# Performance work log

Measured on AMD Instinct MI355X. Metric: run time of the kernel, lower is better.

Reference implementation:

```python
import jax, jax.numpy as jnp
import numpy as np

C = 1.0          # Poincare ball curvature
NORM_FACTOR = 1.0
EPS = 1e-7
MAX_NORM = (1.0 - 1e-5) / np.sqrt(C)


def _artanh(x):
    x = jnp.clip(x, -1.0 + EPS, 1.0 - EPS)
    return jnp.arctanh(x)


def logmap0(x):
    # tangent vector at origin of Poincare ball (c=C)
    n = jnp.clip(jnp.linalg.norm(x, axis=-1, keepdims=True), EPS, None)
    sc = np.sqrt(C)
    return _artanh(sc * n) * x / (sc * n)


def expmap0(u):
    n = jnp.clip(jnp.linalg.norm(u, axis=-1, keepdims=True), EPS, None)
    sc = np.sqrt(C)
    return jnp.tanh(sc * n) * u / (sc * n)


def proj(x):
    # clip points to stay strictly inside the ball
    n = jnp.clip(jnp.linalg.norm(x, axis=-1, keepdims=True), EPS, None)
    return jnp.where(n > MAX_NORM, x / n * MAX_NORM, x)


def setup_inputs() -> dict:
    key = jax.random.key(0)
    ks = jax.random.split(key, 10)
    B, N, D_IN, D_H, D_LAT, L = 32, 1024, 128, 128, 64, 2
    s_in = 1.0 / np.sqrt(D_IN)
    s_h = 1.0 / np.sqrt(D_H)
    return {
        "node_features": jax.random.normal(ks[0], (B, N, D_IN), jnp.float32),
        "adjacency_matrix": jax.random.uniform(ks[1], (B, N, N), jnp.float32),
        "node_mask": jnp.ones((B, N, 1), jnp.float32),
        "W_embed": jax.random.normal(ks[2], (D_H, D_IN), jnp.float32) * s_in,
        "W_msg": jax.random.normal(ks[3], (L, D_H, D_H), jnp.float32) * s_h,
        "b_msg": jnp.zeros((L, D_H), jnp.float32),
        "W_agg": jax.random.normal(ks[4], (L, D_H, D_H), jnp.float32) * s_h,
        "b_agg": jnp.zeros((L, D_H), jnp.float32),
        "W_proj": jax.random.normal(ks[5], (2 * D_LAT, D_H), jnp.float32) * s_h,
        "b_proj": jnp.zeros((2 * D_LAT,), jnp.float32),
    }


def reference(node_features, adjacency_matrix, node_mask,
              W_embed, W_msg, b_msg, W_agg, b_agg, W_proj, b_proj):
    # feature embedding (bias-free linear, weights live on the manifold);
    # map to the Poincare ball
    h = jnp.einsum('bnd,hd->bnh', node_features, W_embed)
    x = proj(expmap0(h))

    num_layers = W_msg.shape[0]
    for l in range(num_layers):  # small fixed layer count
        t = logmap0(x)                                   # [B,N,D]
        m = t @ W_msg[l] + b_msg[l]                      # message transform
        agg = jnp.einsum('bij,bjd->bid', adjacency_matrix, m) / NORM_FACTOR
        agg = agg @ W_agg[l] + b_agg[l]                  # aggregation transform
        t = jax.nn.relu(m + agg)                         # tangent-space activation
        x = proj(expmap0(t))

    tangent = logmap0(x)                                 # final logmap0 in encode()
    mean_logvar = tangent @ W_proj.T + b_proj            # [B,N,2*latent]
    return mean_logvar * node_mask
```

## Files before the change

### kernel.cpp

```cpp
#include <hip/hip_runtime.h>
#include <hip/hip_bf16.h>

typedef __bf16 bf16;
typedef __bf16 bf16x8 __attribute__((ext_vector_type(8)));
typedef float  floatx4 __attribute__((ext_vector_type(4)));

#define EPSF    1e-7f
#define MAXNORM 0.99999f
#define TS_LD   136

__device__ __forceinline__ float hyp_scale(float ss) {
    float n  = sqrtf(ss);
    float nh = fmaxf(n, EPSF);
    float s1 = tanhf(nh) / nh;
    float nx = s1 * n;
    if (nx > MAXNORM) { s1 *= MAXNORM / nx; nx = MAXNORM; }
    float nx2 = fmaxf(nx, EPSF);
    return (atanhf(nx2) / nx2) * s1;
}

__device__ __forceinline__ bf16x8 cvt8(float4 a, float4 b) {
    bf16x8 r;
    r[0] = (bf16)a.x; r[1] = (bf16)a.y; r[2] = (bf16)a.z; r[3] = (bf16)a.w;
    r[4] = (bf16)b.x; r[5] = (bf16)b.y; r[6] = (bf16)b.z; r[7] = (bf16)b.w;
    return r;
}

__device__ __forceinline__ int sw128(int row, int k) {
    return row * 128 + (((k >> 3) ^ (row & 15)) << 3) + (k & 7);
}
__device__ __forceinline__ int sw64(int row, int k) {
    return row * 64 + (((k >> 3) ^ (row & 7)) << 3) + (k & 7);
}

__device__ __forceinline__ void gl_lds16(const void* g, void* l) {
    __builtin_amdgcn_global_load_lds(
        (__attribute__((address_space(1))) unsigned int*)(g),
        (__attribute__((address_space(3))) unsigned int*)(l), 16, 0, 0);
}


__global__ __launch_bounds__(256) void pack_adj(
    const float* __restrict__ Adj, bf16* __restrict__ AdjB)
{
    __shared__ __align__(16) bf16 Ls[4096 * 8];
    const int tid = threadIdx.x, bp = blockIdx.x;
    const int bmt = bp >> 2, q = bp & 3;
    const float* src = Adj + ((size_t)bmt << 17) + ((size_t)q << 15);

    #pragma unroll
    for (int i = 0; i < 16; ++i) {
        int gi = i * 256 + tid;
        int row = gi >> 7, gcol = gi & 127;
        int kk = gcol >> 3, gp = gcol & 7;
        const float4* p = reinterpret_cast<const float4*>(src + ((size_t)gi << 3));
        float4 v0 = p[0], v1 = p[1];
        int gpp = gp ^ (row & 7);
        *reinterpret_cast<bf16x8*>(&Ls[((kk * 32 + row) * 8 + gpp) * 8]) = cvt8(v0, v1);
    }
    __syncthreads();

    bf16* dst = AdjB + ((size_t)bmt << 17);
    #pragma unroll
    for (int i = 0; i < 16; ++i) {
        int go = i * 256 + tid;
        int kk = go >> 8, rem = go & 255;
        *reinterpret_cast<bf16x8*>(&dst[((((size_t)kk << 10) + (q << 8) + rem)) << 3]) =
            *reinterpret_cast<const bf16x8*>(&Ls[go * 8]);
    }
}

__global__ __launch_bounds__(256) void embed_msg(
    const float* __restrict__ X, const float* __restrict__ Wemb,
    const float* __restrict__ Wmsg, const float* __restrict__ bmsg,
    bf16* __restrict__ M, bf16* __restrict__ MT)
{
    __shared__ __align__(16) bf16 Xs[128 * 128];
    __shared__ __align__(16) bf16 Ws[128 * 128];
    __shared__ __align__(16) bf16 W2[128 * 128];
    __shared__ __align__(16) bf16 Ts[128 * TS_LD];
    const int tid = threadIdx.x, bx = blockIdx.x;

    {
        const float4* Xg = reinterpret_cast<const float4*>(X + (size_t)bx * 16384);
        #pragma unroll
        for (int i = 0; i < 8; ++i) {
            int g = tid + i * 256, row = g >> 4, gc = g & 15;
            float4 v0 = Xg[2 * g], v1 = Xg[2 * g + 1];
            *reinterpret_cast<bf16x8*>(&Xs[row * 128 + ((gc ^ (row & 15)) << 3)]) = cvt8(v0, v1);
        }
    }
    {
        const float4* Wg = reinterpret_cast<const float4*>(Wemb);
        #pragma unroll
        for (int i = 0; i < 8; ++i) {
            int g = tid + i * 256, row = g >> 4, gc = g & 15;
            float4 v0 = Wg[2 * g], v1 = Wg[2 * g + 1];
            *reinterpret_cast<bf16x8*>(&Ws[row * 128 + ((gc ^ (row & 15)) << 3)]) = cvt8(v0, v1);
        }
    }
    {
        const int c0 = (tid & 15) * 8;
        #pragma unroll
        for (int rr = 0; rr < 8; ++rr) {
            int r = (tid >> 4) * 8 + rr;
            const float4* p = reinterpret_cast<const float4*>(Wmsg + r * 128 + c0);
            float4 v0 = p[0], v1 = p[1];
            float vv[8] = {v0.x, v0.y, v0.z, v0.w, v1.x, v1.y, v1.z, v1.w};
            #pragma unroll
            for (int j = 0; j < 8; ++j) {
                int n = c0 + j;
                W2[n * 128 + (((r >> 3) ^ (n & 15)) << 3) + (r & 7)] = (bf16)vv[j];
            }
        }
    }
    __syncthreads();

    const int lane = tid & 63, wv = tid >> 6, n16 = lane & 15, quad = lane >> 4;
    const int rbase = wv * 32;

    floatx4 acc[2][8];
    #pragma unroll
    for (int a = 0; a < 2; ++a)
        #pragma unroll
        for (int c = 0; c < 8; ++c) acc[a][c] = (floatx4){0.f, 0.f, 0.f, 0.f};
    #pragma unroll
    for (int kc = 0; kc < 4; ++kc) {
        int k0 = kc * 32 + quad * 8;
        bf16x8 a0 = *reinterpret_cast<const bf16x8*>(&Xs[sw128(rbase + n16, k0)]);
        bf16x8 a1 = *reinterpret_cast<const bf16x8*>(&Xs[sw128(rbase + 16 + n16, k0)]);
        #pragma unroll
        for (int ct = 0; ct < 8; ++ct) {
            bf16x8 b = *reinterpret_cast<const bf16x8*>(&Ws[sw128(ct * 16 + n16, k0)]);
            acc[0][ct] = __builtin_amdgcn_mfma_f32_16x16x32_bf16(a0, b, acc[0][ct], 0, 0, 0);
            acc[1][ct] = __builtin_amdgcn_mfma_f32_16x16x32_bf16(a1, b, acc[1][ct], 0, 0, 0);
        }
    }
    #pragma unroll
    for (int rt = 0; rt < 2; ++rt) {
        #pragma unroll
        for (int r = 0; r < 4; ++r) {
            int row = rbase + rt * 16 + quad * 4 + r;
            float u[8], ss = 0.f;
            #pragma unroll
            for (int ct = 0; ct < 8; ++ct) { u[ct] = acc[rt][ct][r]; ss += u[ct] * u[ct]; }
            #pragma unroll
            for (int off = 1; off < 16; off <<= 1) ss += __shfl_xor(ss, off);
            float sc = hyp_scale(ss);
            #pragma unroll
            for (int ct = 0; ct < 8; ++ct)
                Ts[row * TS_LD + ct * 16 + n16] = (bf16)(u[ct] * sc);
        }
    }
    __syncthreads();

    floatx4 acc2[2][8];
    #pragma unroll
    for (int a = 0; a < 2; ++a)
        #pragma unroll
        for (int c = 0; c < 8; ++c) acc2[a][c] = (floatx4){0.f, 0.f, 0.f, 0.f};
    #pragma unroll
    for (int kc = 0; kc < 4; ++kc) {
        int k0 = kc * 32 + quad * 8;
        bf16x8 a0 = *reinterpret_cast<const bf16x8*>(&Ts[(rbase + n16) * TS_LD + k0]);
        bf16x8 a1 = *reinterpret_cast<const bf16x8*>(&Ts[(rbase + 16 + n16) * TS_LD + k0]);
        #pragma unroll
        for (int ct = 0; ct < 8; ++ct) {
            bf16x8 b = *reinterpret_cast<const bf16x8*>(&W2[sw128(ct * 16 + n16, k0)]);
            acc2[0][ct] = __builtin_amdgcn_mfma_f32_16x16x32_bf16(a0, b, acc2[0][ct], 0, 0, 0);
            acc2[1][ct] = __builtin_amdgcn_mfma_f32_16x16x32_bf16(a1, b, acc2[1][ct], 0, 0, 0);
        }
    }
    float bv[8];
    #pragma unroll
    for (int ct = 0; ct < 8; ++ct) bv[ct] = bmsg[ct * 16 + n16];
    #pragma unroll
    for (int rt = 0; rt < 2; ++rt) {
        #pragma unroll
        for (int r = 0; r < 4; ++r) {
            int lrow = rbase + rt * 16 + quad * 4 + r;
            size_t grow = (size_t)bx * 128 + lrow;
            #pragma unroll
            for (int ct = 0; ct < 8; ++ct) {
                int col = ct * 16 + n16;
                bf16 o = (bf16)(acc2[rt][ct][r] + bv[ct]);
                M[grow * 128 + col] = o;
                Ts[lrow * TS_LD + col] = o;
            }
        }
    }
    __syncthreads();
    {
        const size_t mtb = (((size_t)(bx >> 3) * 16 + (size_t)(bx & 7) * 2) << 10);
        #pragma unroll
        for (int i = 0; i < 8; ++i) {
            int g = i * 256 + tid;
            int n = g & 127, rest = g >> 7, gp = rest & 7, kkl = rest >> 3;
            int k0 = kkl * 64 + ((gp ^ (n & 7)) << 3);
            bf16x8 v;
            #pragma unroll
            for (int j = 0; j < 8; ++j) v[j] = Ts[(k0 + j) * TS_LD + n];
            size_t go = ((size_t)kkl << 10) + (n << 3) + gp;
            *reinterpret_cast<bf16x8*>(MT + ((mtb + go) << 3)) = v;
        }
    }
}

template <int LAST>
__global__ __launch_bounds__(512) void adj_fast(
    const bf16* __restrict__ AdjB, const bf16* __restrict__ MT,
    const bf16* __restrict__ Mprev,
    const float* __restrict__ Wagg, const float* __restrict__ bagg,
    const float* __restrict__ W2f,  const float* __restrict__ b2,
    const float* __restrict__ Mask,
    bf16* __restrict__ Mout, bf16* __restrict__ MTout, float* __restrict__ Out)
{
    __shared__ __align__(16) bf16 smem[6 * 128 * 64];
    __shared__ __align__(16) bf16 Ts[128 * TS_LD];

    const int tid = threadIdx.x, bid = blockIdx.x;
    const int mt = bid >> 5, b = bid & 31;
    const bf16* Ab = AdjB + ((size_t)(b * 8 + mt) << 17);
    const bf16* Bg = MT + ((size_t)b << 17);

    const int lane = tid & 63, wv = tid >> 6, n16 = lane & 15, quad = lane >> 4;
    const int wr = (wv >> 2) * 64, wc = (wv & 3) * 32;

    bf16* As[3] = { smem,         smem + 8192,  smem + 16384 };
    bf16* Bs[3] = { smem + 24576, smem + 32768, smem + 40960 };

    floatx4 acc[4][2];
    #pragma unroll
    for (int a = 0; a < 4; ++a)
        #pragma unroll
        for (int c = 0; c < 2; ++c) acc[a][c] = (floatx4){0.f, 0.f, 0.f, 0.f};

    auto stage = [&](int kk, bf16* Adst, bf16* Bdst) {
        const bf16* at = Ab + ((size_t)kk << 13);
        const bf16* bt = Bg + ((size_t)kk << 13);
        #pragma unroll
        for (int j = 0; j < 2; ++j) {
            int base = wv * 128 + j * 64;
            gl_lds16(at + (size_t)(base + lane) * 8, Adst + base * 8);
            gl_lds16(bt + (size_t)(base + lane) * 8, Bdst + base * 8);
        }
    };

    stage(0, As[0], Bs[0]);
    stage(1, As[1], Bs[1]);
    #pragma unroll
    for (int p = 0; p < 16; ++p) {
        if (p < 15) asm volatile("s_waitcnt vmcnt(4)" ::: "memory");
        else        asm volatile("s_waitcnt vmcnt(0)" ::: "memory");
        __builtin_amdgcn_s_barrier();
        __builtin_amdgcn_sched_barrier(0);
        if (p + 2 < 16) stage(p + 2, As[(p + 2) % 3], Bs[(p + 2) % 3]);
        const bf16* Acur = As[p % 3];
        const bf16* Bcur = Bs[p % 3];
        #pragma unroll
        for (int kc = 0; kc < 2; ++kc) {
            int ko = kc * 32 + quad * 8;
            bf16x8 a[4], bb[2];
            #pragma unroll
            for (int rt = 0; rt < 4; ++rt)
                a[rt] = *reinterpret_cast<const bf16x8*>(&Acur[sw64(wr + rt * 16 + n16, ko)]);
            #pragma unroll
            for (int ct = 0; ct < 2; ++ct)
                bb[ct] = *reinterpret_cast<const bf16x8*>(&Bcur[sw64(wc + ct * 16 + n16, ko)]);
            __builtin_amdgcn_s_setprio(1);
            #pragma unroll
            for (int rt = 0; rt < 4; ++rt)
                #pragma unroll
                for (int ct = 0; ct < 2; ++ct)
                    acc[rt][ct] = __builtin_amdgcn_mfma_f32_16x16x32_bf16(a[rt], bb[ct], acc[rt][ct], 0, 0, 0);
            __builtin_amdgcn_s_setprio(0);
        }
    }
    __syncthreads();

    #pragma unroll
    for (int rt = 0; rt < 4; ++rt)
        #pragma unroll
        for (int ct = 0; ct < 2; ++ct)
            #pragma unroll
            for (int r = 0; r < 4; ++r) {
                int row = wr + rt * 16 + quad * 4 + r, col = wc + ct * 16 + n16;
                Ts[row * TS_LD + col] = (bf16)acc[rt][ct][r];
            }

    bf16* Wa = smem;
    bf16* W2 = smem + 128 * 128;
    {
        const int c0 = (tid & 15) * 8;
        #pragma unroll
        for (int rr = 0; rr < 4; ++rr) {
            int r = (tid >> 4) * 4 + rr;
            const float4* p = reinterpret_cast<const float4*>(Wagg + r * 128 + c0);
            float4 v0 = p[0], v1 = p[1];
            float vv[8] = {v0.x, v0.y, v0.z, v0.w, v1.x, v1.y, v1.z, v1.w};
            #pragma unroll
            for (int j = 0; j < 8; ++j) {
                int n = c0 + j;
                Wa[n * 128 + (((r >> 3) ^ (n & 15)) << 3) + (r & 7)] = (bf16)vv[j];
            }
        }
    }
    if (LAST) {
        const float4* Wg = reinterpret_cast<const float4*>(W2f);
        #pragma unroll
        for (int i = 0; i < 4; ++i) {
            int g = tid + i * 512, row = g >> 4, gc = g & 15;
            float4 v0 = Wg[2 * g], v1 = Wg[2 * g + 1];
            *reinterpret_cast<bf16x8*>(&W2[row * 128 + ((gc ^ (row & 15)) << 3)]) = cvt8(v0, v1);
        }
    } else {
        const int c0 = (tid & 15) * 8;
        #pragma unroll
        for (int rr = 0; rr < 4; ++rr) {
            int r = (tid >> 4) * 4 + rr;
            const float4* p = reinterpret_cast<const float4*>(W2f + r * 128 + c0);
            float4 v0 = p[0], v1 = p[1];
            float vv[8] = {v0.x, v0.y, v0.z, v0.w, v1.x, v1.y, v1.z, v1.w};
            #pragma unroll
            for (int j = 0; j < 8; ++j) {
                int n = c0 + j;
                W2[n * 128 + (((r >> 3) ^ (n & 15)) << 3) + (r & 7)] = (bf16)vv[j];
            }
        }
    }
    __syncthreads();

    const int rbase = wv * 16;
    const size_t growbase = (size_t)b * 1024 + (size_t)mt * 128;
    floatx4 acc2[8];
    #pragma unroll
    for (int c = 0; c < 8; ++c) acc2[c] = (floatx4){0.f, 0.f, 0.f, 0.f};
    #pragma unroll
    for (int kc = 0; kc < 4; ++kc) {
        int k0 = kc * 32 + quad * 8;
        bf16x8 a = *reinterpret_cast<const bf16x8*>(&Ts[(rbase + n16) * TS_LD + k0]);
        #pragma unroll
        for (int ct = 0; ct < 8; ++ct) {
            bf16x8 bb = *reinterpret_cast<const bf16x8*>(&Wa[sw128(ct * 16 + n16, k0)]);
            acc2[ct] = __builtin_amdgcn_mfma_f32_16x16x32_bf16(a, bb, acc2[ct], 0, 0, 0);
        }
    }
    {
        float bva[8];
        #pragma unroll
        for (int ct = 0; ct < 8; ++ct) bva[ct] = bagg[ct * 16 + n16];
        #pragma unroll
        for (int r = 0; r < 4; ++r) {
            int row = rbase + quad * 4 + r;
            size_t grow = growbase + row;
            float u[8], ss = 0.f;
            #pragma unroll
            for (int ct = 0; ct < 8; ++ct) {
                u[ct] = fmaxf(acc2[ct][r] + bva[ct] + (float)Mprev[grow * 128 + ct * 16 + n16], 0.f);
                ss += u[ct] * u[ct];
            }
            #pragma unroll
            for (int off = 1; off < 16; off <<= 1) ss += __shfl_xor(ss, off);
            float sc = hyp_scale(ss);
            #pragma unroll
            for (int ct = 0; ct < 8; ++ct)
                Ts[row * TS_LD + ct * 16 + n16] = (bf16)(u[ct] * sc);
        }
    }

    floatx4 acc3[8];
    #pragma unroll
    for (int c = 0; c < 8; ++c) acc3[c] = (floatx4){0.f, 0.f, 0.f, 0.f};
    #pragma unroll
    for (int kc = 0; kc < 4; ++kc) {
        int k0 = kc * 32 + quad * 8;
        bf16x8 a = *reinterpret_cast<const bf16x8*>(&Ts[(rbase + n16) * TS_LD + k0]);
        #pragma unroll
        for (int ct = 0; ct < 8; ++ct) {
            bf16x8 bb = *reinterpret_cast<const bf16x8*>(&W2[sw128(ct * 16 + n16, k0)]);
            acc3[ct] = __builtin_amdgcn_mfma_f32_16x16x32_bf16(a, bb, acc3[ct], 0, 0, 0);
        }
    }
    float bv2[8];
    #pragma unroll
    for (int ct = 0; ct < 8; ++ct) bv2[ct] = b2[ct * 16 + n16];
    #pragma unroll
    for (int r = 0; r < 4; ++r) {
        int row = rbase + quad * 4 + r;
        size_t grow = growbase + row;
        if (LAST) {
            float mk = Mask[grow];
            #pragma unroll
            for (int ct = 0; ct < 8; ++ct)
                Out[grow * 128 + ct * 16 + n16] = (acc3[ct][r] + bv2[ct]) * mk;
        } else {
            #pragma unroll
            for (int ct = 0; ct < 8; ++ct) {
                int col = ct * 16 + n16;
                bf16 o = (bf16)(acc3[ct][r] + bv2[ct]);
                Mout[grow * 128 + col] = o;
                Ts[row * TS_LD + col] = o;
            }
        }
    }
    if (!LAST) {
        __syncthreads();
        const size_t mtb = (((size_t)b * 16 + (size_t)mt * 2) << 10);
        #pragma unroll
        for (int i = 0; i < 4; ++i) {
            int g = i * 512 + tid;
            int n = g & 127, rest = g >> 7, gp = rest & 7, kkl = rest >> 3;
            int k0 = kkl * 64 + ((gp ^ (n & 7)) << 3);
            bf16x8 v;
            #pragma unroll
            for (int j = 0; j < 8; ++j) v[j] = Ts[(k0 + j) * TS_LD + n];
            size_t go = ((size_t)kkl << 10) + (n << 3) + gp;
            *reinterpret_cast<bf16x8*>(MTout + ((mtb + go) << 3)) = v;
        }
    }
}

__global__ __launch_bounds__(256) void embed_msg_legacy(
    const float* __restrict__ X, const float* __restrict__ Wemb,
    const float* __restrict__ Wmsg, const float* __restrict__ bmsg,
    bf16* __restrict__ M, bf16* __restrict__ MT)
{
    __shared__ __align__(16) bf16 Xs[128 * 128];
    __shared__ __align__(16) bf16 Ws[128 * 128];
    __shared__ __align__(16) bf16 W2[128 * 128];
    __shared__ __align__(16) bf16 Ts[128 * TS_LD];
    const int tid = threadIdx.x, bx = blockIdx.x;

    {
        const float4* Xg = reinterpret_cast<const float4*>(X + (size_t)bx * 16384);
        #pragma unroll
        for (int i = 0; i < 8; ++i) {
            int g = tid + i * 256, row = g >> 4, gc = g & 15;
            float4 v0 = Xg[2 * g], v1 = Xg[2 * g + 1];
            *reinterpret_cast<bf16x8*>(&Xs[row * 128 + ((gc ^ (row & 15)) << 3)]) = cvt8(v0, v1);
        }
    }
    {
        const float4* Wg = reinterpret_cast<const float4*>(Wemb);
        #pragma unroll
        for (int i = 0; i < 8; ++i) {
            int g = tid + i * 256, row = g >> 4, gc = g & 15;
            float4 v0 = Wg[2 * g], v1 = Wg[2 * g + 1];
            *reinterpret_cast<bf16x8*>(&Ws[row * 128 + ((gc ^ (row & 15)) << 3)]) = cvt8(v0, v1);
        }
    }
    {
        const int c0 = (tid & 15) * 8;
        #pragma unroll
        for (int rr = 0; rr < 8; ++rr) {
            int r = (tid >> 4) * 8 + rr;
            const float4* p = reinterpret_cast<const float4*>(Wmsg + r * 128 + c0);
            float4 v0 = p[0], v1 = p[1];
            float vv[8] = {v0.x, v0.y, v0.z, v0.w, v1.x, v1.y, v1.z, v1.w};
            #pragma unroll
            for (int j = 0; j < 8; ++j) {
                int n = c0 + j;
                W2[n * 128 + (((r >> 3) ^ (n & 15)) << 3) + (r & 7)] = (bf16)vv[j];
            }
        }
    }
    __syncthreads();

    const int lane = tid & 63, wv = tid >> 6, n16 = lane & 15, quad = lane >> 4;
    const int rbase = wv * 32;

    floatx4 acc[2][8];
    #pragma unroll
    for (int a = 0; a < 2; ++a)
        #pragma unroll
        for (int c = 0; c < 8; ++c) acc[a][c] = (floatx4){0.f, 0.f, 0.f, 0.f};
    #pragma unroll
    for (int kc = 0; kc < 4; ++kc) {
        int k0 = kc * 32 + quad * 8;
        bf16x8 a0 = *reinterpret_cast<const bf16x8*>(&Xs[sw128(rbase + n16, k0)]);
        bf16x8 a1 = *reinterpret_cast<const bf16x8*>(&Xs[sw128(rbase + 16 + n16, k0)]);
        #pragma unroll
        for (int ct = 0; ct < 8; ++ct) {
            bf16x8 b = *reinterpret_cast<const bf16x8*>(&Ws[sw128(ct * 16 + n16, k0)]);
            acc[0][ct] = __builtin_amdgcn_mfma_f32_16x16x32_bf16(a0, b, acc[0][ct], 0, 0, 0);
            acc[1][ct] = __builtin_amdgcn_mfma_f32_16x16x32_bf16(a1, b, acc[1][ct], 0, 0, 0);
        }
    }
    #pragma unroll
    for (int rt = 0; rt < 2; ++rt) {
        #pragma unroll
        for (int r = 0; r < 4; ++r) {
            int row = rbase + rt * 16 + quad * 4 + r;
            float u[8], ss = 0.f;
            #pragma unroll
            for (int ct = 0; ct < 8; ++ct) { u[ct] = acc[rt][ct][r]; ss += u[ct] * u[ct]; }
            #pragma unroll
            for (int off = 1; off < 16; off <<= 1) ss += __shfl_xor(ss, off);
            float sc = hyp_scale(ss);
            #pragma unroll
            for (int ct = 0; ct < 8; ++ct)
                Ts[row * TS_LD + ct * 16 + n16] = (bf16)(u[ct] * sc);
        }
    }
    __syncthreads();

    floatx4 acc2[2][8];
    #pragma unroll
    for (int a = 0; a < 2; ++a)
        #pragma unroll
        for (int c = 0; c < 8; ++c) acc2[a][c] = (floatx4){0.f, 0.f, 0.f, 0.f};
    #pragma unroll
    for (int kc = 0; kc < 4; ++kc) {
        int k0 = kc * 32 + quad * 8;
        bf16x8 a0 = *reinterpret_cast<const bf16x8*>(&Ts[(rbase + n16) * TS_LD + k0]);
        bf16x8 a1 = *reinterpret_cast<const bf16x8*>(&Ts[(rbase + 16 + n16) * TS_LD + k0]);
        #pragma unroll
        for (int ct = 0; ct < 8; ++ct) {
            bf16x8 b = *reinterpret_cast<const bf16x8*>(&W2[sw128(ct * 16 + n16, k0)]);
            acc2[0][ct] = __builtin_amdgcn_mfma_f32_16x16x32_bf16(a0, b, acc2[0][ct], 0, 0, 0);
            acc2[1][ct] = __builtin_amdgcn_mfma_f32_16x16x32_bf16(a1, b, acc2[1][ct], 0, 0, 0);
        }
    }
    float bv[8];
    #pragma unroll
    for (int ct = 0; ct < 8; ++ct) bv[ct] = bmsg[ct * 16 + n16];
    #pragma unroll
    for (int rt = 0; rt < 2; ++rt) {
        #pragma unroll
        for (int r = 0; r < 4; ++r) {
            int lrow = rbase + rt * 16 + quad * 4 + r;
            size_t grow = (size_t)bx * 128 + lrow;
            #pragma unroll
            for (int ct = 0; ct < 8; ++ct) {
                bf16 o = (bf16)(acc2[rt][ct][r] + bv[ct]);
                M[grow * 128 + ct * 16 + n16] = o;
                MT[((grow >> 10) * 128 + ct * 16 + n16) * 1024 + (grow & 1023)] = o;
            }
        }
    }
}

template <int LAST>
__global__ __launch_bounds__(512) void adj_fused(
    const float* __restrict__ Adj, const bf16* __restrict__ MT,
    const bf16* __restrict__ Mprev,
    const float* __restrict__ Wagg, const float* __restrict__ bagg,
    const float* __restrict__ W2f,  const float* __restrict__ b2,
    const float* __restrict__ Mask,
    bf16* __restrict__ Mout, bf16* __restrict__ MTout, float* __restrict__ Out)
{
    __shared__ __align__(16) bf16 smem[4 * 128 * 64];
    __shared__ __align__(16) bf16 Ts[128 * TS_LD];
    bf16* As0 = smem;
    bf16* As1 = smem + 128 * 64;
    bf16* Bs0 = smem + 2 * 128 * 64;
    bf16* Bs1 = smem + 3 * 128 * 64;

    const int tid = threadIdx.x, bid = blockIdx.x;
    const int mt = bid >> 5, b = bid & 31;
    const float* Ag = Adj + ((size_t)b << 20) + ((size_t)mt << 17);
    const bf16*  Bg = MT  + ((size_t)b << 17);

    const int lane = tid & 63, wv = tid >> 6, n16 = lane & 15, quad = lane >> 4;
    const int wr = (wv >> 2) * 64, wc = (wv & 3) * 32;

    const int kk0 = (bid * 5 + (bid >> 5)) & 15;

    floatx4 acc[4][2];
    #pragma unroll
    for (int a = 0; a < 4; ++a)
        #pragma unroll
        for (int c = 0; c < 2; ++c) acc[a][c] = (floatx4){0.f, 0.f, 0.f, 0.f};

    float4 pa[2][2]; bf16x8 pb[2];
    auto load_regs = [&](int kk) {
        #pragma unroll
        for (int i = 0; i < 2; ++i) {
            int g = tid + i * 512, row = g >> 3, gc = g & 7;
            const float4* pA = reinterpret_cast<const float4*>(
                Ag + (size_t)row * 1024 + kk * 64 + gc * 8);
            pa[i][0] = pA[0]; pa[i][1] = pA[1];
            pb[i] = *reinterpret_cast<const bf16x8*>(Bg + (size_t)row * 1024 + kk * 64 + gc * 8);
        }
    };
    auto store_lds = [&](bf16* A, bf16* B) {
        #pragma unroll
        for (int i = 0; i < 2; ++i) {
            int g = tid + i * 512, row = g >> 3, gc = g & 7;
            *reinterpret_cast<bf16x8*>(&A[row * 64 + ((gc ^ (row & 7)) << 3)]) = cvt8(pa[i][0], pa[i][1]);
            *reinterpret_cast<bf16x8*>(&B[row * 64 + ((gc ^ (row & 7)) << 3)]) = pb[i];
        }
    };

    load_regs(kk0);
    store_lds(As0, Bs0);
    for (int p = 0; p < 16; ++p) {
        bf16* Acur = (p & 1) ? As1 : As0;
        bf16* Bcur = (p & 1) ? Bs1 : Bs0;
        bf16* Anxt = (p & 1) ? As0 : As1;
        bf16* Bnxt = (p & 1) ? Bs0 : Bs1;
        __syncthreads();
        if (p < 15) load_regs((p + 1 + kk0) & 15);
        #pragma unroll
        for (int kc = 0; kc < 2; ++kc) {
            int ko = kc * 32 + quad * 8;
            bf16x8 a[4], bb[2];
            #pragma unroll
            for (int rt = 0; rt < 4; ++rt)
                a[rt] = *reinterpret_cast<const bf16x8*>(&Acur[sw64(wr + rt * 16 + n16, ko)]);
            #pragma unroll
            for (int ct = 0; ct < 2; ++ct)
                bb[ct] = *reinterpret_cast<const bf16x8*>(&Bcur[sw64(wc + ct * 16 + n16, ko)]);
            #pragma unroll
            for (int rt = 0; rt < 4; ++rt)
                #pragma unroll
                for (int ct = 0; ct < 2; ++ct)
                    acc[rt][ct] = __builtin_amdgcn_mfma_f32_16x16x32_bf16(a[rt], bb[ct], acc[rt][ct], 0, 0, 0);
        }
        if (p < 15) store_lds(Anxt, Bnxt);
    }
    __syncthreads();

    #pragma unroll
    for (int rt = 0; rt < 4; ++rt)
        #pragma unroll
        for (int ct = 0; ct < 2; ++ct)
            #pragma unroll
            for (int r = 0; r < 4; ++r) {
                int row = wr + rt * 16 + quad * 4 + r, col = wc + ct * 16 + n16;
                Ts[row * TS_LD + col] = (bf16)acc[rt][ct][r];
            }

    bf16* Wa = smem;
    bf16* W2 = smem + 128 * 128;
    {
        const int c0 = (tid & 15) * 8;
        #pragma unroll
        for (int rr = 0; rr < 4; ++rr) {
            int r = (tid >> 4) * 4 + rr;
            const float4* p = reinterpret_cast<const float4*>(Wagg + r * 128 + c0);
            float4 v0 = p[0], v1 = p[1];
            float vv[8] = {v0.x, v0.y, v0.z, v0.w, v1.x, v1.y, v1.z, v1.w};
            #pragma unroll
            for (int j = 0; j < 8; ++j) {
                int n = c0 + j;
                Wa[n * 128 + (((r >> 3) ^ (n & 15)) << 3) + (r & 7)] = (bf16)vv[j];
            }
        }
    }
    if (LAST) {
        const float4* Wg = reinterpret_cast<const float4*>(W2f);
        #pragma unroll
        for (int i = 0; i < 4; ++i) {
            int g = tid + i * 512, row = g >> 4, gc = g & 15;
            float4 v0 = Wg[2 * g], v1 = Wg[2 * g + 1];
            *reinterpret_cast<bf16x8*>(&W2[row * 128 + ((gc ^ (row & 15)) << 3)]) = cvt8(v0, v1);
        }
    } else {
        const int c0 = (tid & 15) * 8;
        #pragma unroll
        for (int rr = 0; rr < 4; ++rr) {
            int r = (tid >> 4) * 4 + rr;
            const float4* p = reinterpret_cast<const float4*>(W2f + r * 128 + c0);
            float4 v0 = p[0], v1 = p[1];
            float vv[8] = {v0.x, v0.y, v0.z, v0.w, v1.x, v1.y, v1.z, v1.w};
            #pragma unroll
            for (int j = 0; j < 8; ++j) {
                int n = c0 + j;
                W2[n * 128 + (((r >> 3) ^ (n & 15)) << 3) + (r & 7)] = (bf16)vv[j];
            }
        }
    }
    __syncthreads();

    const int rbase = wv * 16;
    const size_t growbase = (size_t)b * 1024 + (size_t)mt * 128;
    floatx4 acc2[8];
    #pragma unroll
    for (int c = 0; c < 8; ++c) acc2[c] = (floatx4){0.f, 0.f, 0.f, 0.f};
    #pragma unroll
    for (int kc = 0; kc < 4; ++kc) {
        int k0 = kc * 32 + quad * 8;
        bf16x8 a = *reinterpret_cast<const bf16x8*>(&Ts[(rbase + n16) * TS_LD + k0]);
        #pragma unroll
        for (int ct = 0; ct < 8; ++ct) {
            bf16x8 bb = *reinterpret_cast<const bf16x8*>(&Wa[sw128(ct * 16 + n16, k0)]);
            acc2[ct] = __builtin_amdgcn_mfma_f32_16x16x32_bf16(a, bb, acc2[ct], 0, 0, 0);
        }
    }
    {
        float bva[8];
        #pragma unroll
        for (int ct = 0; ct < 8; ++ct) bva[ct] = bagg[ct * 16 + n16];
        #pragma unroll
        for (int r = 0; r < 4; ++r) {
            int row = rbase + quad * 4 + r;
            size_t grow = growbase + row;
            float u[8], ss = 0.f;
            #pragma unroll
            for (int ct = 0; ct < 8; ++ct) {
                u[ct] = fmaxf(acc2[ct][r] + bva[ct] + (float)Mprev[grow * 128 + ct * 16 + n16], 0.f);
                ss += u[ct] * u[ct];
            }
            #pragma unroll
            for (int off = 1; off < 16; off <<= 1) ss += __shfl_xor(ss, off);
            float sc = hyp_scale(ss);
            #pragma unroll
            for (int ct = 0; ct < 8; ++ct)
                Ts[row * TS_LD + ct * 16 + n16] = (bf16)(u[ct] * sc);
        }
    }

    floatx4 acc3[8];
    #pragma unroll
    for (int c = 0; c < 8; ++c) acc3[c] = (floatx4){0.f, 0.f, 0.f, 0.f};
    #pragma unroll
    for (int kc = 0; kc < 4; ++kc) {
        int k0 = kc * 32 + quad * 8;
        bf16x8 a = *reinterpret_cast<const bf16x8*>(&Ts[(rbase + n16) * TS_LD + k0]);
        #pragma unroll
        for (int ct = 0; ct < 8; ++ct) {
            bf16x8 bb = *reinterpret_cast<const bf16x8*>(&W2[sw128(ct * 16 + n16, k0)]);
            acc3[ct] = __builtin_amdgcn_mfma_f32_16x16x32_bf16(a, bb, acc3[ct], 0, 0, 0);
        }
    }
    float bv2[8];
    #pragma unroll
    for (int ct = 0; ct < 8; ++ct) bv2[ct] = b2[ct * 16 + n16];
    #pragma unroll
    for (int r = 0; r < 4; ++r) {
        int row = rbase + quad * 4 + r;
        size_t grow = growbase + row;
        if (LAST) {
            float mk = Mask[grow];
            #pragma unroll
            for (int ct = 0; ct < 8; ++ct)
                Out[grow * 128 + ct * 16 + n16] = (acc3[ct][r] + bv2[ct]) * mk;
        } else {
            #pragma unroll
            for (int ct = 0; ct < 8; ++ct) {
                bf16 o = (bf16)(acc3[ct][r] + bv2[ct]);
                Mout[grow * 128 + ct * 16 + n16] = o;
                MTout[((grow >> 10) * 128 + ct * 16 + n16) * 1024 + (grow & 1023)] = o;
            }
        }
    }
}

extern "C" void kernel_launch(void* const* d_in, const int* in_sizes, int n_in,
                              void* d_out, int out_size, void* d_ws, size_t ws_size,
                              hipStream_t stream)
{
    const float* X    = (const float*)d_in[0];
    const float* Adj  = (const float*)d_in[1];
    const float* Mask = (const float*)d_in[2];
    const float* Wemb = (const float*)d_in[3];
    const float* Wmsg = (const float*)d_in[4];
    const float* bmsg = (const float*)d_in[5];
    const float* Wagg = (const float*)d_in[6];
    const float* bagg = (const float*)d_in[7];
    const float* Wprj = (const float*)d_in[8];
    const float* bprj = (const float*)d_in[9];
    float* out = (float*)d_out;

    const size_t BN = 32768;
    bf16* m0   = (bf16*)d_ws;
    bf16* m0T  = m0  + BN * 128;
    bf16* m1   = m0T + BN * 128;
    bf16* m1T  = m1  + BN * 128;
    bf16* AdjB = m1T + BN * 128;

    const size_t need = (4 * BN * 128 + (size_t)33554432) * sizeof(bf16);

    if (ws_size >= need) {
        pack_adj<<<1024, 256, 0, stream>>>(Adj, AdjB);
        embed_msg<<<256, 256, 0, stream>>>(X, Wemb, Wmsg, bmsg, m0, m0T);
        adj_fast<0><<<256, 512, 0, stream>>>(AdjB, m0T, m0, Wagg, bagg,
                                             Wmsg + 16384, bmsg + 128, nullptr,
                                             m1, m1T, nullptr);
        adj_fast<1><<<256, 512, 0, stream>>>(AdjB, m1T, m1, Wagg + 16384, bagg + 128,
                                             Wprj, bprj, Mask,
                                             nullptr, nullptr, out);
    } else {
        embed_msg_legacy<<<256, 256, 0, stream>>>(X, Wemb, Wmsg, bmsg, m0, m0T);
        adj_fused<0><<<256, 512, 0, stream>>>(Adj, m0T, m0, Wagg, bagg,
                                              Wmsg + 16384, bmsg + 128, nullptr,
                                              m1, m1T, nullptr);
        adj_fused<1><<<256, 512, 0, stream>>>(Adj, m1T, m1, Wagg + 16384, bagg + 128,
                                              Wprj, bprj, Mask,
                                              nullptr, nullptr, out);
    }
}
```

Before: 335.4 us.

## Split adjacency row tiles in half to double grid and rework transpose staging

adj_fast now processes 64-row tiles instead of 128, launching 512 blocks instead of 256 so more CUs have work on the 256-CU device. Shared memory is shrunk and reused across phases, and the epilogue GEMMs run on only half the waves. The transposed MT output is staged through an XOR-swizzled dim-major buffer so it can be read with vector loads instead of scalar gathers, in both embed_msg and adj_fast. In exchange, the B operand (MT) is loaded twice across the two halves and the epilogue leaves half the waves idle.

```diff
diff --git a/kernel.cpp b/kernel.cpp
--- a/kernel.cpp
+++ b/kernel.cpp
@@ -181,27 +181,33 @@
             int lrow = rbase + rt * 16 + quad * 4 + r;
             size_t grow = (size_t)bx * 128 + lrow;
             #pragma unroll
+            for (int ct = 0; ct < 8; ++ct)
+                M[grow * 128 + ct * 16 + n16] = (bf16)(acc2[rt][ct][r] + bv[ct]);
+        }
+    }
+    __syncthreads();
+    bf16* Ts2 = W2;
+    #pragma unroll
+    for (int rt = 0; rt < 2; ++rt) {
+        #pragma unroll
+        for (int r = 0; r < 4; ++r) {
+            int lrow = rbase + rt * 16 + quad * 4 + r;
+            #pragma unroll
             for (int ct = 0; ct < 8; ++ct) {
-                int col = ct * 16 + n16;
-                bf16 o = (bf16)(acc2[rt][ct][r] + bv[ct]);
-                M[grow * 128 + col] = o;
-                Ts[lrow * TS_LD + col] = o;
-            }
-        }
-    }
-    __syncthreads();
-    {
-        const size_t mtb = (((size_t)(bx >> 3) * 16 + (size_t)(bx & 7) * 2) << 10);
+                int dim = ct * 16 + n16;
+                Ts2[dim * 128 + (lrow ^ ((dim & 7) << 3))] = (bf16)(acc2[rt][ct][r] + bv[ct]);
+            }
+        }
+    }
+    __syncthreads();
+    {
+        const size_t tb = (((size_t)(bx >> 3) * 16 + (size_t)(bx & 7) * 2) << 10);
         #pragma unroll
         for (int i = 0; i < 8; ++i) {
             int g = i * 256 + tid;
-            int n = g & 127, rest = g >> 7, gp = rest & 7, kkl = rest >> 3;
-            int k0 = kkl * 64 + ((gp ^ (n & 7)) << 3);
-            bf16x8 v;
-            #pragma unroll
-            for (int j = 0; j < 8; ++j) v[j] = Ts[(k0 + j) * TS_LD + n];
-            size_t go = ((size_t)kkl << 10) + (n << 3) + gp;
-            *reinterpret_cast<bf16x8*>(MT + ((mtb + go) << 3)) = v;
+            int gp = g & 7, n = (g >> 3) & 127, kkl = g >> 10;
+            bf16x8 v = *reinterpret_cast<const bf16x8*>(&Ts2[n * 128 + kkl * 64 + gp * 8]);
+            *reinterpret_cast<bf16x8*>(MT + ((tb + (size_t)g) << 3)) = v;
         }
     }
 }
@@ -215,33 +221,32 @@
     const float* __restrict__ Mask,
     bf16* __restrict__ Mout, bf16* __restrict__ MTout, float* __restrict__ Out)
 {
-    __shared__ __align__(16) bf16 smem[6 * 128 * 64];
-    __shared__ __align__(16) bf16 Ts[128 * TS_LD];
+    __shared__ __align__(16) bf16 smem[36864];
+    bf16* As[3] = { smem, smem + 4096, smem + 8192 };
+    bf16* Bs[3] = { smem + 12288, smem + 20480, smem + 28672 };
 
     const int tid = threadIdx.x, bid = blockIdx.x;
-    const int mt = bid >> 5, b = bid & 31;
+    const int h = bid >> 8, inner = bid & 255;
+    const int mt = inner >> 5, b = inner & 31;
     const bf16* Ab = AdjB + ((size_t)(b * 8 + mt) << 17);
     const bf16* Bg = MT + ((size_t)b << 17);
 
     const int lane = tid & 63, wv = tid >> 6, n16 = lane & 15, quad = lane >> 4;
-    const int wr = (wv >> 2) * 64, wc = (wv & 3) * 32;
-
-    bf16* As[3] = { smem,         smem + 8192,  smem + 16384 };
-    bf16* Bs[3] = { smem + 24576, smem + 32768, smem + 40960 };
-
-    floatx4 acc[4][2];
-    #pragma unroll
-    for (int a = 0; a < 4; ++a)
+    const int wr = (wv >> 2) * 32, wc = (wv & 3) * 32;
+
+    floatx4 acc[2][2];
+    #pragma unroll
+    for (int a = 0; a < 2; ++a)
         #pragma unroll
         for (int c = 0; c < 2; ++c) acc[a][c] = (floatx4){0.f, 0.f, 0.f, 0.f};
 
     auto stage = [&](int kk, bf16* Adst, bf16* Bdst) {
-        const bf16* at = Ab + ((size_t)kk << 13);
+        const bf16* at = Ab + ((size_t)kk << 13) + ((size_t)h << 12);
         const bf16* bt = Bg + ((size_t)kk << 13);
+        gl_lds16(at + (size_t)(wv * 64 + lane) * 8, Adst + (wv * 64) * 8);
         #pragma unroll
         for (int j = 0; j < 2; ++j) {
             int base = wv * 128 + j * 64;
-            gl_lds16(at + (size_t)(base + lane) * 8, Adst + base * 8);
             gl_lds16(bt + (size_t)(base + lane) * 8, Bdst + base * 8);
         }
     };
@@ -250,7 +255,7 @@
     stage(1, As[1], Bs[1]);
     #pragma unroll
     for (int p = 0; p < 16; ++p) {
-        if (p < 15) asm volatile("s_waitcnt vmcnt(4)" ::: "memory");
+        if (p < 15) asm volatile("s_waitcnt vmcnt(3)" ::: "memory");
         else        asm volatile("s_waitcnt vmcnt(0)" ::: "memory");
         __builtin_amdgcn_s_barrier();
         __builtin_amdgcn_sched_barrier(0);
@@ -260,16 +265,16 @@
         #pragma unroll
         for (int kc = 0; kc < 2; ++kc) {
             int ko = kc * 32 + quad * 8;
-            bf16x8 a[4], bb[2];
-            #pragma unroll
-            for (int rt = 0; rt < 4; ++rt)
+            bf16x8 a[2], bb[2];
+            #pragma unroll
+            for (int rt = 0; rt < 2; ++rt)
                 a[rt] = *reinterpret_cast<const bf16x8*>(&Acur[sw64(wr + rt * 16 + n16, ko)]);
             #pragma unroll
             for (int ct = 0; ct < 2; ++ct)
                 bb[ct] = *reinterpret_cast<const bf16x8*>(&Bcur[sw64(wc + ct * 16 + n16, ko)]);
             __builtin_amdgcn_s_setprio(1);
             #pragma unroll
-            for (int rt = 0; rt < 4; ++rt)
+            for (int rt = 0; rt < 2; ++rt)
                 #pragma unroll
                 for (int ct = 0; ct < 2; ++ct)
                     acc[rt][ct] = __builtin_amdgcn_mfma_f32_16x16x32_bf16(a[rt], bb[ct], acc[rt][ct], 0, 0, 0);
@@ -278,8 +283,12 @@
     }
     __syncthreads();
 
-    #pragma unroll
-    for (int rt = 0; rt < 4; ++rt)
+    bf16* Ts  = smem;
+    bf16* Wa  = smem + 12288;
+    bf16* Ts2 = smem + 28672;
+
+    #pragma unroll
+    for (int rt = 0; rt < 2; ++rt)
         #pragma unroll
         for (int ct = 0; ct < 2; ++ct)
             #pragma unroll
@@ -287,9 +296,6 @@
                 int row = wr + rt * 16 + quad * 4 + r, col = wc + ct * 16 + n16;
                 Ts[row * TS_LD + col] = (bf16)acc[rt][ct][r];
             }
-
-    bf16* Wa = smem;
-    bf16* W2 = smem + 128 * 128;
     {
         const int c0 = (tid & 15) * 8;
         #pragma unroll
@@ -305,13 +311,54 @@
             }
         }
     }
+    __syncthreads();
+
+    const int rbase = (wv & 3) * 16;
+    const size_t growbase = (size_t)b * 1024 + (size_t)mt * 128 + (size_t)h * 64;
+    floatx4 acc2[8];
+    #pragma unroll
+    for (int c = 0; c < 8; ++c) acc2[c] = (floatx4){0.f, 0.f, 0.f, 0.f};
+    if (wv < 4) {
+        #pragma unroll
+        for (int kc = 0; kc < 4; ++kc) {
+            int k0 = kc * 32 + quad * 8;
+            bf16x8 a = *reinterpret_cast<const bf16x8*>(&Ts[(rbase + n16) * TS_LD + k0]);
+            #pragma unroll
+            for (int ct = 0; ct < 8; ++ct) {
+                bf16x8 bb = *reinterpret_cast<const bf16x8*>(&Wa[sw128(ct * 16 + n16, k0)]);
+                acc2[ct] = __builtin_amdgcn_mfma_f32_16x16x32_bf16(a, bb, acc2[ct], 0, 0, 0);
+            }
+        }
+        float bva[8];
+        #pragma unroll
+        for (int ct = 0; ct < 8; ++ct) bva[ct] = bagg[ct * 16 + n16];
+        #pragma unroll
+        for (int r = 0; r < 4; ++r) {
+            int row = rbase + quad * 4 + r;
+            size_t grow = growbase + row;
+            float u[8], ss = 0.f;
+            #pragma unroll
+            for (int ct = 0; ct < 8; ++ct) {
+                u[ct] = fmaxf(acc2[ct][r] + bva[ct] + (float)Mprev[grow * 128 + ct * 16 + n16], 0.f);
+                ss += u[ct] * u[ct];
+            }
+            #pragma unroll
+            for (int off = 1; off < 16; off <<= 1) ss += __shfl_xor(ss, off);
+            float sc = hyp_scale(ss);
+            #pragma unroll
+            for (int ct = 0; ct < 8; ++ct)
+                Ts[row * TS_LD + ct * 16 + n16] = (bf16)(u[ct] * sc);
+        }
+    }
+    __syncthreads();
+
     if (LAST) {
         const float4* Wg = reinterpret_cast<const float4*>(W2f);
         #pragma unroll
         for (int i = 0; i < 4; ++i) {
             int g = tid + i * 512, row = g >> 4, gc = g & 15;
             float4 v0 = Wg[2 * g], v1 = Wg[2 * g + 1];
-            *reinterpret_cast<bf16x8*>(&W2[row * 128 + ((gc ^ (row & 15)) << 3)]) = cvt8(v0, v1);
+            *reinterpret_cast<bf16x8*>(&Wa[row * 128 + ((gc ^ (row & 15)) << 3)]) = cvt8(v0, v1);
         }
     } else {
         const int c0 = (tid & 15) * 8;
@@ -324,98 +371,58 @@
             #pragma unroll
             for (int j = 0; j < 8; ++j) {
                 int n = c0 + j;
-                W2[n * 128 + (((r >> 3) ^ (n & 15)) << 3) + (r & 7)] = (bf16)vv[j];
-            }
-        }
-    }
-    __syncthreads();
-
-    const int rbase = wv * 16;
-    const size_t growbase = (size_t)b * 1024 + (size_t)mt * 128;
-    floatx4 acc2[8];
-    #pragma unroll
-    for (int c = 0; c < 8; ++c) acc2[c] = (floatx4){0.f, 0.f, 0.f, 0.f};
-    #pragma unroll
-    for (int kc = 0; kc < 4; ++kc) {
-        int k0 = kc * 32 + quad * 8;
-        bf16x8 a = *reinterpret_cast<const bf16x8*>(&Ts[(rbase + n16) * TS_LD + k0]);
-        #pragma unroll
-        for (int ct = 0; ct < 8; ++ct) {
-            bf16x8 bb = *reinterpret_cast<const bf16x8*>(&Wa[sw128(ct * 16 + n16, k0)]);
-            acc2[ct] = __builtin_amdgcn_mfma_f32_16x16x32_bf16(a, bb, acc2[ct], 0, 0, 0);
-        }
-    }
-    {
-        float bva[8];
-        #pragma unroll
-        for (int ct = 0; ct < 8; ++ct) bva[ct] = bagg[ct * 16 + n16];
+                Wa[n * 128 + (((r >> 3) ^ (n & 15)) << 3) + (r & 7)] = (bf16)vv[j];
+            }
+        }
+    }
+    __syncthreads();
+
+    floatx4 acc3[8];
+    #pragma unroll
+    for (int c = 0; c < 8; ++c) acc3[c] = (floatx4){0.f, 0.f, 0.f, 0.f};
+    if (wv < 4) {
+        #pragma unroll
+        for (int kc = 0; kc < 4; ++kc) {
+            int k0 = kc * 32 + quad * 8;
+            bf16x8 a = *reinterpret_cast<const bf16x8*>(&Ts[(rbase + n16) * TS_LD + k0]);
+            #pragma unroll
+            for (int ct = 0; ct < 8; ++ct) {
+                bf16x8 bb = *reinterpret_cast<const bf16x8*>(&Wa[sw128(ct * 16 + n16, k0)]);
+                acc3[ct] = __builtin_amdgcn_mfma_f32_16x16x32_bf16(a, bb, acc3[ct], 0, 0, 0);
+            }
+        }
+        float bv2[8];
+        #pragma unroll
+        for (int ct = 0; ct < 8; ++ct) bv2[ct] = b2[ct * 16 + n16];
         #pragma unroll
         for (int r = 0; r < 4; ++r) {
             int row = rbase + quad * 4 + r;
             size_t grow = growbase + row;
-            float u[8], ss = 0.f;
-            #pragma unroll
-            for (int ct = 0; ct < 8; ++ct) {
-                u[ct] = fmaxf(acc2[ct][r] + bva[ct] + (float)Mprev[grow * 128 + ct * 16 + n16], 0.f);
-                ss += u[ct] * u[ct];
-            }
-            #pragma unroll
-            for (int off = 1; off < 16; off <<= 1) ss += __shfl_xor(ss, off);
-            float sc = hyp_scale(ss);
-            #pragma unroll
-            for (int ct = 0; ct < 8; ++ct)
-                Ts[row * TS_LD + ct * 16 + n16] = (bf16)(u[ct] * sc);
-        }
-    }
-
-    floatx4 acc3[8];
-    #pragma unroll
-    for (int c = 0; c < 8; ++c) acc3[c] = (floatx4){0.f, 0.f, 0.f, 0.f};
-    #pragma unroll
-    for (int kc = 0; kc < 4; ++kc) {
-        int k0 = kc * 32 + quad * 8;
-        bf16x8 a = *reinterpret_cast<const bf16x8*>(&Ts[(rbase + n16) * TS_LD + k0]);
-        #pragma unroll
-        for (int ct = 0; ct < 8; ++ct) {
-            bf16x8 bb = *reinterpret_cast<const bf16x8*>(&W2[sw128(ct * 16 + n16, k0)]);
-            acc3[ct] = __builtin_amdgcn_mfma_f32_16x16x32_bf16(a, bb, acc3[ct], 0, 0, 0);
-        }
-    }
-    float bv2[8];
-    #pragma unroll
-    for (int ct = 0; ct < 8; ++ct) bv2[ct] = b2[ct * 16 + n16];
-    #pragma unroll
-    for (int r = 0; r < 4; ++r) {
-        int row = rbase + quad * 4 + r;
-        size_t grow = growbase + row;
-        if (LAST) {
-            float mk = Mask[grow];
-            #pragma unroll
-            for (int ct = 0; ct < 8; ++ct)
-                Out[grow * 128 + ct * 16 + n16] = (acc3[ct][r] + bv2[ct]) * mk;
-        } else {
-            #pragma unroll
-            for (int ct = 0; ct < 8; ++ct) {
-                int col = ct * 16 + n16;
-                bf16 o = (bf16)(acc3[ct][r] + bv2[ct]);
-                Mout[grow * 128 + col] = o;
-                Ts[row * TS_LD + col] = o;
+            if (LAST) {
+                float mk = Mask[grow];
+                #pragma unroll
+                for (int ct = 0; ct < 8; ++ct)
+                    Out[grow * 128 + ct * 16 + n16] = (acc3[ct][r] + bv2[ct]) * mk;
+            } else {
+                #pragma unroll
+                for (int ct = 0; ct < 8; ++ct) {
+                    int dim = ct * 16 + n16;
+                    bf16 o = (bf16)(acc3[ct][r] + bv2[ct]);
+                    Mout[grow * 128 + dim] = o;
+                    Ts2[dim * 64 + (row ^ ((dim & 7) << 3))] = o;
+                }
             }
         }
     }
     if (!LAST) {
         __syncthreads();
-        const size_t mtb = (((size_t)b * 16 + (size_t)mt * 2) << 10);
-        #pragma unroll
-        for (int i = 0; i < 4; ++i) {
+        const size_t tb = (((size_t)b * 16 + (size_t)(mt * 2 + h)) << 10);
+        #pragma unroll
+        for (int i = 0; i < 2; ++i) {
             int g = i * 512 + tid;
-            int n = g & 127, rest = g >> 7, gp = rest & 7, kkl = rest >> 3;
-            int k0 = kkl * 64 + ((gp ^ (n & 7)) << 3);
-            bf16x8 v;
-            #pragma unroll
-            for (int j = 0; j < 8; ++j) v[j] = Ts[(k0 + j) * TS_LD + n];
-            size_t go = ((size_t)kkl << 10) + (n << 3) + gp;
-            *reinterpret_cast<bf16x8*>(MTout + ((mtb + go) << 3)) = v;
+            int gp = g & 7, n = g >> 3;
+            bf16x8 v = *reinterpret_cast<const bf16x8*>(&Ts2[n * 64 + gp * 8]);
+            *reinterpret_cast<bf16x8*>(MTout + ((tb + (size_t)g) << 3)) = v;
         }
     }
 }
@@ -775,10 +782,10 @@
     if (ws_size >= need) {
         pack_adj<<<1024, 256, 0, stream>>>(Adj, AdjB);
         embed_msg<<<256, 256, 0, stream>>>(X, Wemb, Wmsg, bmsg, m0, m0T);
-        adj_fast<0><<<256, 512, 0, stream>>>(AdjB, m0T, m0, Wagg, bagg,
+        adj_fast<0><<<512, 512, 0, stream>>>(AdjB, m0T, m0, Wagg, bagg,
                                              Wmsg + 16384, bmsg + 128, nullptr,
                                              m1, m1T, nullptr);
-        adj_fast<1><<<256, 512, 0, stream>>>(AdjB, m1T, m1, Wagg + 16384, bagg + 128,
+        adj_fast<1><<<512, 512, 0, stream>>>(AdjB, m1T, m1, Wagg + 16384, bagg + 128,
                                              Wprj, bprj, Mask,
                                              nullptr, nullptr, out);
     } else {
```

Result: faster. 313.9 us (-6.4%).
